# Performance work log

Measured on AMD Instinct MI355X. Metric: run time of the kernel, lower is better.

The kernel has to match this reference:

```python
import jax, jax.numpy as jnp
import numpy as np

B, T, D = 1, 4096, 2048
NUM_HEADS, NUM_KV_HEADS, HEAD_DIM = 16, 8, 128
QUERY_PRE_ATTN_SCALAR = HEAD_DIM ** -0.5
SOFT_CAP = 50.0
WINDOW = 1024
ROPE_BASE = 10000.0
ROPE_SCALE = 1.0
K_MASK = -2.3819763e+38


def apply_rope(x, positions, head_dim, max_wavelength=ROPE_BASE, scale_factor=ROPE_SCALE):
    # x: [B, T, N, H], positions: [B, T]
    fraction = 2.0 * jnp.arange(head_dim // 2, dtype=jnp.float32) / head_dim
    timescale = max_wavelength ** fraction  # [H/2]
    sinusoid = positions[..., None].astype(jnp.float32) / timescale  # [B, T, H/2]
    sinusoid = (sinusoid / scale_factor)[..., None, :]  # [B, T, 1, H/2]
    sin, cos = jnp.sin(sinusoid), jnp.cos(sinusoid)
    first, second = jnp.split(x, 2, axis=-1)
    out = jnp.concatenate([first * cos - second * sin,
                           second * cos + first * sin], axis=-1)
    return out.astype(x.dtype)


def setup_inputs() -> dict:
    key = jax.random.key(0)
    ks = jax.random.split(key, 4)
    x = jax.random.normal(ks[0], (B, T, D), dtype=jnp.float32)
    segment_pos = jnp.broadcast_to(jnp.arange(T, dtype=jnp.int32), (B, T))
    # causal mask [B, T, S]
    attn_mask = jnp.broadcast_to(
        jnp.tril(jnp.ones((T, T), dtype=jnp.bool_)), (B, T, T))
    q_w = jax.random.normal(ks[1], (NUM_HEADS, D, HEAD_DIM), dtype=jnp.float32) * 0.02
    kv_w = jax.random.normal(ks[2], (2, NUM_KV_HEADS, D, HEAD_DIM), dtype=jnp.float32) * 0.02
    o_w = jax.random.normal(ks[3], (NUM_HEADS, HEAD_DIM, D), dtype=jnp.float32) * 0.02
    return {"x": x, "segment_pos": segment_pos, "attn_mask": attn_mask,
            "q_w": q_w, "kv_w": kv_w, "o_w": o_w}


def reference(x, segment_pos, attn_mask, q_w, kv_w, o_w):
    # Projections (GQA: separate q and kv einsums)
    q = jnp.einsum('BTD,NDH->BTNH', x, q_w)          # [B,T,N,H]
    k = jnp.einsum('BSD,KDH->BSKH', x, kv_w[0])      # [B,S,K,H]
    v = jnp.einsum('BSD,KDH->BSKH', x, kv_w[1])      # [B,S,K,H]

    q = apply_rope(q, segment_pos, HEAD_DIM)
    q = q * QUERY_PRE_ATTN_SCALAR
    k = apply_rope(k, segment_pos, HEAD_DIM)

    num_groups = NUM_HEADS // NUM_KV_HEADS
    qg = q.reshape(B, T, NUM_KV_HEADS, num_groups, HEAD_DIM)
    logits = jnp.einsum('BTKGH,BSKH->BTKGS', qg, k)
    logits = logits.reshape(B, T, NUM_HEADS, -1)     # [B,T,N,S]

    # soft cap
    logits = jnp.tanh(logits / SOFT_CAP) * SOFT_CAP

    # sliding-window mask combined with causal mask
    all_ones = jnp.ones_like(attn_mask)
    sliding = jnp.triu(all_ones, -WINDOW + 1) * jnp.tril(all_ones, WINDOW - 1)
    mask = sliding * attn_mask                       # [B,T,S] bool

    padded = jnp.where(mask[:, :, None, :], logits, K_MASK)
    probs = jax.nn.softmax(padded, axis=-1).astype(k.dtype)

    probs_g = probs.reshape(B, T, NUM_KV_HEADS, num_groups, -1)
    encoded = jnp.einsum('BTKGS,BSKH->BTKGH', probs_g, v)
    encoded = encoded.reshape(B, T, NUM_HEADS, HEAD_DIM)

    attn_output = jnp.einsum('BTNH,NHD->BTD', encoded, o_w)
    return attn_output
```

## Files before the change

kernel.cpp:

```cpp
#include <hip/hip_runtime.h>
#include <hip/hip_bf16.h>
#include <math.h>

typedef __attribute__((ext_vector_type(8))) short short8;
typedef __attribute__((ext_vector_type(8))) unsigned short ushort8;
typedef __attribute__((ext_vector_type(4))) float f32x4;

#define T_SEQ 4096
#define D_MODEL 2048
#define N_HEADS 16
#define N_KV 8
#define HEAD_DIM 128
#define QSCALE 0.08838834764831845f

__device__ __forceinline__ float bf2f(unsigned short u) {
  union { unsigned int i; float f; } x; x.i = ((unsigned int)u) << 16; return x.f;
}
__device__ __forceinline__ unsigned short f2bf(float f) {
  union { float f; unsigned int i; } x; x.f = f;
  unsigned int i = x.i;
  unsigned int r = i + 0x7fffu + ((i >> 16) & 1u);
  return (unsigned short)(r >> 16);
}

__global__ __launch_bounds__(256) void cvt_x_kernel(const float* __restrict__ x,
                                                    unsigned short* __restrict__ xb) {
  int idx = blockIdx.x * 256 + threadIdx.x;
  const float4* p = reinterpret_cast<const float4*>(x) + (size_t)idx * 2;
  float4 a = p[0], b = p[1];
  ushort8 o;
  o[0] = f2bf(a.x); o[1] = f2bf(a.y); o[2] = f2bf(a.z); o[3] = f2bf(a.w);
  o[4] = f2bf(b.x); o[5] = f2bf(b.y); o[6] = f2bf(b.z); o[7] = f2bf(b.w);
  reinterpret_cast<ushort8*>(xb)[idx] = o;
}

__global__ __launch_bounds__(256) void rope_table_kernel(const int* __restrict__ segpos,
                                                         float2* __restrict__ tab) {
  int idx = blockIdx.x * 256 + threadIdx.x;
  int t = idx >> 6, i = idx & 63;
  float pos = (float)segpos[t];
  float ts = powf(10000.f, (float)(2 * i) / 128.f);
  float ang = pos / ts;
  tab[idx] = make_float2(sinf(ang), cosf(ang));
}

__global__ __launch_bounds__(256) void transpose_f32_bf16_kernel(const float* __restrict__ src,
                                                                 unsigned short* __restrict__ dst,
                                                                 int sstride, int dstride,
                                                                 long sBatch, long dBatch) {
  __shared__ float tile[32][33];
  long b = blockIdx.z;
  src += b * sBatch; dst += b * dBatch;
  int c0 = blockIdx.x * 32, r0 = blockIdx.y * 32;
  int tx = threadIdx.x & 31, ty = threadIdx.x >> 5;
#pragma unroll
  for (int i = 0; i < 4; ++i)
    tile[ty + i * 8][tx] = src[(size_t)(r0 + ty + i * 8) * sstride + c0 + tx];
  __syncthreads();
#pragma unroll
  for (int i = 0; i < 4; ++i)
    dst[(size_t)(c0 + ty + i * 8) * dstride + r0 + tx] = f2bf(tile[tx][ty + i * 8]);
}

__global__ __launch_bounds__(256) void transpose_bf16_kernel(const unsigned short* __restrict__ src,
                                                             unsigned short* __restrict__ dst,
                                                             int sstride, int dstride,
                                                             long sBatch, long dBatch) {
  __shared__ unsigned short tile[32][33];
  long b = blockIdx.z;
  src += b * sBatch; dst += b * dBatch;
  int c0 = blockIdx.x * 32, r0 = blockIdx.y * 32;
  int tx = threadIdx.x & 31, ty = threadIdx.x >> 5;
#pragma unroll
  for (int i = 0; i < 4; ++i)
    tile[ty + i * 8][tx] = src[(size_t)(r0 + ty + i * 8) * sstride + c0 + tx];
  __syncthreads();
#pragma unroll
  for (int i = 0; i < 4; ++i)
    dst[(size_t)(c0 + ty + i * 8) * dstride + r0 + tx] = tile[tx][ty + i * 8];
}

#define G2L(gp, lp)                                                           \
  __builtin_amdgcn_global_load_lds(                                           \
      (const __attribute__((address_space(1))) void*)(gp),                    \
      (__attribute__((address_space(3))) void*)(lp), 16, 0, 0)

template <int OUT_BF16>
__global__ __launch_bounds__(256) void gemm_bt_kernel(const unsigned short* __restrict__ A,
                                                      const unsigned short* __restrict__ Bt,
                                                      void* __restrict__ Cout,
                                                      int M, int N, int K) {
  __shared__ unsigned short As[2][128 * 64];
  __shared__ unsigned short Bs[2][128 * 64];
  const int tid = threadIdx.x;
  const int lane = tid & 63;
  const int wave = tid >> 6;
  const int lr = lane & 15, lg = lane >> 4;
  const long brow = (long)blockIdx.y * 128, bcol = (long)blockIdx.x * 128;
  const int wr = (wave >> 1) * 64, wc = (wave & 1) * 64;
  f32x4 acc[4][4] = {};

  const int er = tid >> 3;
  const int ecs = ((tid & 7) * 8) ^ ((er & 7) << 3);
  const unsigned short* gA = A + (size_t)(brow + er) * K + ecs;
  const unsigned short* gB = Bt + (size_t)(bcol + er) * K + ecs;
  const int ldst = wave * 512;

#define STAGE(buf, k0)                                                        \
  {                                                                           \
    _Pragma("unroll")                                                         \
    for (int i = 0; i < 4; ++i) {                                             \
      G2L(gA + (size_t)i * 32 * K + (k0), &As[buf][i * 2048 + ldst]);         \
      G2L(gB + (size_t)i * 32 * K + (k0), &Bs[buf][i * 2048 + ldst]);         \
    }                                                                         \
  }

  const int nk = K >> 6;
  STAGE(0, 0);
  asm volatile("s_waitcnt vmcnt(0)" ::: "memory");
  __syncthreads();
  int cur = 0;
  const int swr = (lr & 7) << 3;
  for (int t = 0; t < nk; ++t) {
    if (t + 1 < nk) STAGE(cur ^ 1, (t + 1) << 6);
#pragma unroll
    for (int kk = 0; kk < 64; kk += 32) {
      short8 af[4], bfr[4];
#pragma unroll
      for (int m = 0; m < 4; ++m)
        af[m] = *(const short8*)&As[cur][(wr + m * 16 + lr) * 64 + ((kk + lg * 8) ^ swr)];
#pragma unroll
      for (int n = 0; n < 4; ++n)
        bfr[n] = *(const short8*)&Bs[cur][(wc + n * 16 + lr) * 64 + ((kk + lg * 8) ^ swr)];
#pragma unroll
      for (int m = 0; m < 4; ++m)
#pragma unroll
        for (int n = 0; n < 4; ++n)
          acc[m][n] = __builtin_amdgcn_mfma_f32_16x16x32_bf16(af[m], bfr[n], acc[m][n], 0, 0, 0);
    }
    asm volatile("s_waitcnt vmcnt(0)" ::: "memory");
    __syncthreads();
    cur ^= 1;
  }
#undef STAGE

#pragma unroll
  for (int m = 0; m < 4; ++m) {
#pragma unroll
    for (int i = 0; i < 4; ++i) {
      long row = brow + wr + m * 16 + lg * 4 + i;
#pragma unroll
      for (int n = 0; n < 4; ++n) {
        long col = bcol + wc + n * 16 + lr;
        if (OUT_BF16)
          ((unsigned short*)Cout)[row * N + col] = f2bf(acc[m][n][i]);
        else
          ((float*)Cout)[row * N + col] = acc[m][n][i];
      }
    }
  }
}

__global__ __launch_bounds__(256) void rope_apply_kernel(const unsigned short* __restrict__ raw,
                                                         const float2* __restrict__ tab,
                                                         unsigned short* __restrict__ Qb,
                                                         unsigned short* __restrict__ Kb) {
  int gid = blockIdx.x * 256 + threadIdx.x;
  int j = gid & 7;
  int rem = gid >> 3;
  int hs = rem % 24;
  int t = rem / 24;
  int i0 = j * 8;
  float sv[8], cv[8];
  const float2* tp = tab + t * 64 + i0;
#pragma unroll
  for (int q = 0; q < 8; ++q) { float2 sc2 = tp[q]; sv[q] = sc2.x; cv[q] = sc2.y; }
  if (hs < 16) {
    const unsigned short* p = raw + (size_t)t * 4096 + hs * 128 + i0;
    ushort8 a = *(const ushort8*)p;
    ushort8 b = *(const ushort8*)(p + 64);
    ushort8 o1, o2;
#pragma unroll
    for (int q = 0; q < 8; ++q) {
      float fa = bf2f(a[q]), fb = bf2f(b[q]);
      o1[q] = f2bf((fa * cv[q] - fb * sv[q]) * QSCALE);
      o2[q] = f2bf((fb * cv[q] + fa * sv[q]) * QSCALE);
    }
    unsigned short* qp = Qb + ((size_t)hs * T_SEQ + t) * 128 + i0;
    *(ushort8*)qp = o1;
    *(ushort8*)(qp + 64) = o2;
  } else {
    int kn = hs - 16;
    const unsigned short* p = raw + (size_t)t * 4096 + 2048 + kn * 128 + i0;
    ushort8 a = *(const ushort8*)p;
    ushort8 b = *(const ushort8*)(p + 64);
    ushort8 o1, o2;
#pragma unroll
    for (int q = 0; q < 8; ++q) {
      float fa = bf2f(a[q]), fb = bf2f(b[q]);
      o1[q] = f2bf(fa * cv[q] - fb * sv[q]);
      o2[q] = f2bf(fb * cv[q] + fa * sv[q]);
    }
    unsigned short* kp = Kb + ((size_t)kn * T_SEQ + t) * 128 + i0;
    *(ushort8*)kp = o1;
    *(ushort8*)(kp + 64) = o2;
  }
}

__global__ __launch_bounds__(512) void attn_kernel(const unsigned short* __restrict__ Qb,
                                                   const unsigned short* __restrict__ Kb,
                                                   const unsigned short* __restrict__ Vt,
                                                   unsigned short* __restrict__ enc) {
  __shared__ unsigned short Ks[64][128];
  __shared__ unsigned short Vs[128][64];
  __shared__ unsigned short Ps[8][16][66];
  int lin = blockIdx.y * 32 + blockIdx.x;
  lin = (lin & 7) * 64 + (lin >> 3);
  const int h = lin >> 5;
  const int qb0 = (lin & 31) * 128;
  const int kvh = h >> 1;
  const int tid = threadIdx.x, lane = tid & 63, wave = tid >> 6;
  const int qw = qb0 + wave * 16;
  const int lr = lane & 15, lg = lane >> 4;
  const int sw = (lr & 7) << 3;

  short8 aq[4];
  {
    const unsigned short* qp = Qb + ((size_t)h * T_SEQ + qw + lr) * 128 + lg * 8;
#pragma unroll
    for (int c = 0; c < 4; ++c) aq[c] = *(const short8*)(qp + c * 32);
  }
  f32x4 acc[8] = {};
  float lsum[4] = {0.f, 0.f, 0.f, 0.f};

  const int s_lo = (qb0 - 1023) > 0 ? (qb0 - 1023) : 0;
  const int kb_lo = s_lo >> 6, kb_hi = (qb0 + 127) >> 6;

  const int rK = tid >> 4;
  const int cpK = (tid & 15) * 8;
  const int colK = cpK ^ ((rK & 7) << 3);
  const int rV = tid >> 3;
  const int cpV = (tid & 7) * 8;
  const int colV = cpV ^ ((rV & 7) << 3);
  const unsigned short* kgb = Kb + ((size_t)kvh * T_SEQ + rK) * 128 + colK;
  const unsigned short* vgb = Vt + ((size_t)kvh * 128 + rV) * T_SEQ + colV;

  ushort8 kr0, kr1, vr0, vr1;
  {
    const int s0g = kb_lo * 64;
    kr0 = *(const ushort8*)(kgb + (size_t)s0g * 128);
    kr1 = *(const ushort8*)(kgb + (size_t)(s0g + 32) * 128);
    vr0 = *(const ushort8*)(vgb + s0g);
    vr1 = *(const ushort8*)(vgb + (size_t)64 * T_SEQ + s0g);
  }

  for (int kb = kb_lo; kb <= kb_hi; ++kb) {
    const int s0g = kb * 64;
    __syncthreads();
    *(ushort8*)&Ks[rK][cpK] = kr0;
    *(ushort8*)&Ks[rK + 32][cpK] = kr1;
    *(ushort8*)&Vs[rV][cpV] = vr0;
    *(ushort8*)&Vs[rV + 64][cpV] = vr1;
    __syncthreads();
    if (kb < kb_hi) {
      const int sn = s0g + 64;
      kr0 = *(const ushort8*)(kgb + (size_t)sn * 128);
      kr1 = *(const ushort8*)(kgb + (size_t)(sn + 32) * 128);
      vr0 = *(const ushort8*)(vgb + sn);
      vr1 = *(const ushort8*)(vgb + (size_t)64 * T_SEQ + sn);
    }
    if (s0g > qw + 15 || s0g + 63 < qw - 1023) continue;

    f32x4 sv[4] = {};
#pragma unroll
    for (int st = 0; st < 4; ++st) {
      const int krow = st * 16 + lr;
#pragma unroll
      for (int c = 0; c < 4; ++c) {
        short8 b = *(const short8*)&Ks[krow][(c * 32 + lg * 8) ^ sw];
        sv[st] = __builtin_amdgcn_mfma_f32_16x16x32_bf16(aq[c], b, sv[st], 0, 0, 0);
      }
    }
#pragma unroll
    for (int st = 0; st < 4; ++st) {
#pragma unroll
      for (int r = 0; r < 4; ++r) {
        float s = sv[st][r];
        float z2 = s * s * 4.0e-4f;
        float capped = s * (15.f + z2) * __builtin_amdgcn_rcpf(fmaf(z2, 6.f, 15.f));
        float p = __expf(capped);
        int qg = qw + lg * 4 + r;
        int sg = s0g + st * 16 + lr;
        p = ((unsigned)(qg - sg) <= 1023u) ? p : 0.f;
        lsum[r] += p;
        Ps[wave][lg * 4 + r][st * 16 + lr] = f2bf(p);
      }
    }
    short8 pa0 = *(const short8*)&Ps[wave][lr][lg * 8];
    short8 pa1 = *(const short8*)&Ps[wave][lr][32 + lg * 8];
#pragma unroll
    for (int d0 = 0; d0 < 8; ++d0) {
      const int vrow = d0 * 16 + lr;
      short8 bv0 = *(const short8*)&Vs[vrow][(lg * 8) ^ sw];
      short8 bv1 = *(const short8*)&Vs[vrow][(32 + lg * 8) ^ sw];
      acc[d0] = __builtin_amdgcn_mfma_f32_16x16x32_bf16(pa0, bv0, acc[d0], 0, 0, 0);
      acc[d0] = __builtin_amdgcn_mfma_f32_16x16x32_bf16(pa1, bv1, acc[d0], 0, 0, 0);
    }
  }

#pragma unroll
  for (int r = 0; r < 4; ++r) {
    float l = lsum[r];
    l += __shfl_xor(l, 1);
    l += __shfl_xor(l, 2);
    l += __shfl_xor(l, 4);
    l += __shfl_xor(l, 8);
    float inv = __builtin_amdgcn_rcpf(l);
    int row = qw + lg * 4 + r;
    unsigned short* op = enc + (size_t)row * D_MODEL + h * 128 + lr;
#pragma unroll
    for (int d0 = 0; d0 < 8; ++d0) op[d0 * 16] = f2bf(acc[d0][r] * inv);
  }
}

extern "C" void kernel_launch(void* const* d_in, const int* in_sizes, int n_in,
                              void* d_out, int out_size, void* d_ws, size_t ws_size,
                              hipStream_t stream) {
  const float* x = (const float*)d_in[0];
  const int* segpos = (const int*)d_in[1];
  const float* q_w = (const float*)d_in[3];
  const float* kv_w = (const float*)d_in[4];
  const float* o_w = (const float*)d_in[5];
  float* out = (float*)d_out;
  char* ws = (char*)d_ws;

  const size_t OFF_XB = 0;
  const size_t OFF_WT = OFF_XB + 16777216;
  const size_t OFF_RAW = OFF_WT + 16777216;
  const size_t OFF_KB = OFF_RAW + 33554432;
  const size_t OFF_VT = OFF_KB + 8388608;
  const size_t OFF_TAB = OFF_VT + 8388608;
  unsigned short* xb = (unsigned short*)(ws + OFF_XB);
  unsigned short* Wt = (unsigned short*)(ws + OFF_WT);
  unsigned short* raw = (unsigned short*)(ws + OFF_RAW);
  unsigned short* Kb = (unsigned short*)(ws + OFF_KB);
  unsigned short* Vt = (unsigned short*)(ws + OFF_VT);
  float2* tab = (float2*)(ws + OFF_TAB);
  unsigned short* o_wt = xb;
  unsigned short* Qb = Wt;
  unsigned short* enc = raw;

  cvt_x_kernel<<<dim3(4096), dim3(256), 0, stream>>>(x, xb);
  rope_table_kernel<<<dim3(1024), dim3(256), 0, stream>>>(segpos, tab);
  transpose_f32_bf16_kernel<<<dim3(4, 64, 16), dim3(256), 0, stream>>>(
      q_w, Wt, 128, 2048, (long)2048 * 128, (long)128 * 2048);
  transpose_f32_bf16_kernel<<<dim3(4, 64, 16), dim3(256), 0, stream>>>(
      kv_w, Wt + (size_t)2048 * 2048, 128, 2048, (long)2048 * 128, (long)128 * 2048);
  gemm_bt_kernel<1><<<dim3(32, 32), dim3(256), 0, stream>>>(xb, Wt, (void*)raw, 4096, 4096, 2048);
  transpose_f32_bf16_kernel<<<dim3(64, 64, 1), dim3(256), 0, stream>>>(
      o_w, o_wt, 2048, 2048, 0L, 0L);
  rope_apply_kernel<<<dim3(3072), dim3(256), 0, stream>>>(raw, tab, Qb, Kb);
  transpose_bf16_kernel<<<dim3(4, 128, 8), dim3(256), 0, stream>>>(
      raw + 3072, Vt, 4096, 4096, 128L, (long)128 * 4096);
  attn_kernel<<<dim3(32, 16), dim3(512), 0, stream>>>(Qb, Kb, Vt, enc);
  gemm_bt_kernel<0><<<dim3(16, 32), dim3(256), 0, stream>>>(enc, o_wt, (void*)out, 4096, 2048, 2048);
}
```

Measured before the change: 224.5 us.

## Replace 128x128 GEMM with 256x256 tile, 8-wave pipelined GEMM and block swizzle

Replaces the two projection GEMMs with a 256x256-tile kernel of 512 threads, using 128KB dynamic LDS with double buffering. Loads are interleaved with MFMA phases using explicit barriers, vmcnt waits and setprio. Block IDs are swizzled for L2 locality. The goal is higher arithmetic intensity and better latency hiding, at the cost of fewer blocks: 256 and 128 workgroups on 256 CUs, which risks underfilling the GPU for the output projection.

After: 226.9 us. No clear change (+1.0%).

```diff
diff --git a/kernel.cpp b/kernel.cpp
--- a/kernel.cpp
+++ b/kernel.cpp
@@ -84,74 +84,126 @@
   __builtin_amdgcn_global_load_lds(                                           \
       (const __attribute__((address_space(1))) void*)(gp),                    \
       (__attribute__((address_space(3))) void*)(lp), 16, 0, 0)
+#define GBAR() asm volatile("s_barrier" ::: "memory")
+#define VMW(n) asm volatile("s_waitcnt vmcnt(" #n ")" ::: "memory")
 
 template <int OUT_BF16>
-__global__ __launch_bounds__(256) void gemm_bt_kernel(const unsigned short* __restrict__ A,
-                                                      const unsigned short* __restrict__ Bt,
-                                                      void* __restrict__ Cout,
-                                                      int M, int N, int K) {
-  __shared__ unsigned short As[2][128 * 64];
-  __shared__ unsigned short Bs[2][128 * 64];
+__global__ __launch_bounds__(512, 2) void gemm256_kernel(const unsigned short* __restrict__ A,
+                                                         const unsigned short* __restrict__ Bt,
+                                                         void* __restrict__ Cout,
+                                                         int M, int N, int K) {
+  extern __shared__ unsigned short smem[];
+  unsigned short* ldsA = smem;
+  unsigned short* ldsB = smem + 32768;
   const int tid = threadIdx.x;
-  const int lane = tid & 63;
-  const int wave = tid >> 6;
+  const int lane = tid & 63, wave = tid >> 6;
+  const int wm = wave >> 2, wn = wave & 3;
   const int lr = lane & 15, lg = lane >> 4;
-  const long brow = (long)blockIdx.y * 128, bcol = (long)blockIdx.x * 128;
-  const int wr = (wave >> 1) * 64, wc = (wave & 1) * 64;
-  f32x4 acc[4][4] = {};
-
-  const int er = tid >> 3;
-  const int ecs = ((tid & 7) * 8) ^ ((er & 7) << 3);
-  const unsigned short* gA = A + (size_t)(brow + er) * K + ecs;
-  const unsigned short* gB = Bt + (size_t)(bcol + er) * K + ecs;
-  const int ldst = wave * 512;
-
-#define STAGE(buf, k0)                                                        \
-  {                                                                           \
+  const int swz = (lr & 7) << 3;
+  const int c0s = (lg * 8) ^ swz;
+  const int c1s = (32 + lg * 8) ^ swz;
+
+  int id = blockIdx.y * gridDim.x + blockIdx.x;
+  int nb = gridDim.x * gridDim.y;
+  int sw = (id & 7) * (nb >> 3) + (id >> 3);
+  const long brow = (long)(sw / gridDim.x) * 256;
+  const long bcol = (long)(sw % gridDim.x) * 256;
+
+  const unsigned short* Ag = A + brow * K;
+  const unsigned short* Bg = Bt + bcol * K;
+
+  const int r0 = tid >> 3;
+  const int cs = ((tid & 7) * 8) ^ ((r0 & 7) << 3);
+
+#define ST_A(tt, b, a)                                                        \
+  { G2L(Ag + (size_t)((a) * 128 + r0) * K + (size_t)(tt) * 64 + cs,           \
+        ldsA + (b) * 16384 + (a) * 8192 + tid * 8);                           \
+    G2L(Ag + (size_t)((a) * 128 + r0 + 64) * K + (size_t)(tt) * 64 + cs,      \
+        ldsA + (b) * 16384 + (a) * 8192 + 4096 + tid * 8); }
+#define ST_B(tt, b, h)                                                        \
+  { G2L(Bg + (size_t)((h) * 128 + r0) * K + (size_t)(tt) * 64 + cs,           \
+        ldsB + (b) * 16384 + (h) * 8192 + tid * 8);                           \
+    G2L(Bg + (size_t)((h) * 128 + r0 + 64) * K + (size_t)(tt) * 64 + cs,      \
+        ldsB + (b) * 16384 + (h) * 8192 + 4096 + tid * 8); }
+
+  f32x4 acc[8][4] = {};
+  short8 bf[4][2];
+  short8 af[4];
+
+#define RD_B(b)                                                               \
+  { const unsigned short* pb = ldsB + (b) * 16384 + (wn >> 1) * 8192 + (wn & 1) * 4096; \
     _Pragma("unroll")                                                         \
-    for (int i = 0; i < 4; ++i) {                                             \
-      G2L(gA + (size_t)i * 32 * K + (k0), &As[buf][i * 2048 + ldst]);         \
-      G2L(gB + (size_t)i * 32 * K + (k0), &Bs[buf][i * 2048 + ldst]);         \
+    for (int n = 0; n < 4; ++n) {                                             \
+      bf[n][0] = *(const short8*)(pb + (n * 16 + lr) * 64 + c0s);             \
+      bf[n][1] = *(const short8*)(pb + (n * 16 + lr) * 64 + c1s);             \
+    } }
+#define RD_A(b, mb)                                                           \
+  { const unsigned short* pa = ldsA + (b) * 16384 + wm * 8192;                \
+    af[0] = *(const short8*)(pa + ((mb) * 16 + lr) * 64 + c0s);               \
+    af[1] = *(const short8*)(pa + ((mb) * 16 + lr) * 64 + c1s);               \
+    af[2] = *(const short8*)(pa + ((mb) * 16 + 16 + lr) * 64 + c0s);          \
+    af[3] = *(const short8*)(pa + ((mb) * 16 + 16 + lr) * 64 + c1s); }
+#define MFMA2(mb)                                                             \
+  { __builtin_amdgcn_s_setprio(1);                                            \
+    _Pragma("unroll")                                                         \
+    for (int n = 0; n < 4; ++n) {                                             \
+      acc[mb][n]     = __builtin_amdgcn_mfma_f32_16x16x32_bf16(af[0], bf[n][0], acc[mb][n], 0, 0, 0);     \
+      acc[mb][n]     = __builtin_amdgcn_mfma_f32_16x16x32_bf16(af[1], bf[n][1], acc[mb][n], 0, 0, 0);     \
+      acc[mb + 1][n] = __builtin_amdgcn_mfma_f32_16x16x32_bf16(af[2], bf[n][0], acc[mb + 1][n], 0, 0, 0); \
+      acc[mb + 1][n] = __builtin_amdgcn_mfma_f32_16x16x32_bf16(af[3], bf[n][1], acc[mb + 1][n], 0, 0, 0); \
     }                                                                         \
-  }
-
-  const int nk = K >> 6;
-  STAGE(0, 0);
-  asm volatile("s_waitcnt vmcnt(0)" ::: "memory");
-  __syncthreads();
-  int cur = 0;
-  const int swr = (lr & 7) << 3;
-  for (int t = 0; t < nk; ++t) {
-    if (t + 1 < nk) STAGE(cur ^ 1, (t + 1) << 6);
-#pragma unroll
-    for (int kk = 0; kk < 64; kk += 32) {
-      short8 af[4], bfr[4];
-#pragma unroll
-      for (int m = 0; m < 4; ++m)
-        af[m] = *(const short8*)&As[cur][(wr + m * 16 + lr) * 64 + ((kk + lg * 8) ^ swr)];
-#pragma unroll
-      for (int n = 0; n < 4; ++n)
-        bfr[n] = *(const short8*)&Bs[cur][(wc + n * 16 + lr) * 64 + ((kk + lg * 8) ^ swr)];
-#pragma unroll
-      for (int m = 0; m < 4; ++m)
-#pragma unroll
-        for (int n = 0; n < 4; ++n)
-          acc[m][n] = __builtin_amdgcn_mfma_f32_16x16x32_bf16(af[m], bfr[n], acc[m][n], 0, 0, 0);
-    }
-    asm volatile("s_waitcnt vmcnt(0)" ::: "memory");
-    __syncthreads();
-    cur ^= 1;
-  }
-#undef STAGE
-
-#pragma unroll
-  for (int m = 0; m < 4; ++m) {
+    __builtin_amdgcn_s_setprio(0); }
+
+  ST_B(0, 0, 0); ST_B(0, 0, 1); ST_A(0, 0, 0); ST_A(0, 0, 1);
+  ST_B(1, 1, 0); ST_B(1, 1, 1);
+  VMW(4);
+  ST_A(1, 1, 0); ST_A(1, 1, 1);
+  GBAR();
+
+  const int NT = K >> 6;
+  for (int j = 0; j < (NT >> 1); ++j) {
+    const int t2 = 2 * j + 2, t3 = 2 * j + 3;
+    const bool s2 = t2 < NT, s3 = t3 < NT;
+    RD_B(0); RD_A(0, 0);
+    if (s2) ST_B(t2, 0, 0);
+    GBAR(); MFMA2(0); GBAR();
+    RD_A(0, 2);
+    if (s2) ST_B(t2, 0, 1);
+    GBAR(); MFMA2(2); GBAR();
+    RD_A(0, 4);
+    GBAR(); MFMA2(4); GBAR();
+    RD_A(0, 6);
+    if (s2) { VMW(4); ST_A(t2, 0, 0); ST_A(t2, 0, 1); }
+    else    { VMW(0); }
+    GBAR(); MFMA2(6); GBAR();
+    RD_B(1); RD_A(1, 0);
+    if (s3) ST_B(t3, 1, 0);
+    GBAR(); MFMA2(0); GBAR();
+    RD_A(1, 2);
+    if (s3) ST_B(t3, 1, 1);
+    GBAR(); MFMA2(2); GBAR();
+    RD_A(1, 4);
+    GBAR(); MFMA2(4); GBAR();
+    RD_A(1, 6);
+    if (s3) { VMW(4); ST_A(t3, 1, 0); ST_A(t3, 1, 1); }
+    else    { VMW(0); }
+    GBAR(); MFMA2(6); GBAR();
+  }
+
+#undef ST_A
+#undef ST_B
+#undef RD_A
+#undef RD_B
+#undef MFMA2
+
+#pragma unroll
+  for (int m = 0; m < 8; ++m) {
 #pragma unroll
     for (int i = 0; i < 4; ++i) {
-      long row = brow + wr + m * 16 + lg * 4 + i;
+      long row = brow + wm * 128 + m * 16 + lg * 4 + i;
 #pragma unroll
       for (int n = 0; n < 4; ++n) {
-        long col = bcol + wc + n * 16 + lr;
+        long col = bcol + wn * 64 + n * 16 + lr;
         if (OUT_BF16)
           ((unsigned short*)Cout)[row * N + col] = f2bf(acc[m][n][i]);
         else
@@ -350,18 +402,23 @@
   unsigned short* Qb = Wt;
   unsigned short* enc = raw;
 
+  hipFuncSetAttribute((const void*)(gemm256_kernel<1>),
+                      hipFuncAttributeMaxDynamicSharedMemorySize, 131072);
+  hipFuncSetAttribute((const void*)(gemm256_kernel<0>),
+                      hipFuncAttributeMaxDynamicSharedMemorySize, 131072);
+
   cvt_x_kernel<<<dim3(4096), dim3(256), 0, stream>>>(x, xb);
   rope_table_kernel<<<dim3(1024), dim3(256), 0, stream>>>(segpos, tab);
   transpose_f32_bf16_kernel<<<dim3(4, 64, 16), dim3(256), 0, stream>>>(
       q_w, Wt, 128, 2048, (long)2048 * 128, (long)128 * 2048);
   transpose_f32_bf16_kernel<<<dim3(4, 64, 16), dim3(256), 0, stream>>>(
       kv_w, Wt + (size_t)2048 * 2048, 128, 2048, (long)2048 * 128, (long)128 * 2048);
-  gemm_bt_kernel<1><<<dim3(32, 32), dim3(256), 0, stream>>>(xb, Wt, (void*)raw, 4096, 4096, 2048);
+  gemm256_kernel<1><<<dim3(16, 16), dim3(512), 131072, stream>>>(xb, Wt, (void*)raw, 4096, 4096, 2048);
   transpose_f32_bf16_kernel<<<dim3(64, 64, 1), dim3(256), 0, stream>>>(
       o_w, o_wt, 2048, 2048, 0L, 0L);
   rope_apply_kernel<<<dim3(3072), dim3(256), 0, stream>>>(raw, tab, Qb, Kb);
   transpose_bf16_kernel<<<dim3(4, 128, 8), dim3(256), 0, stream>>>(
       raw + 3072, Vt, 4096, 4096, 128L, (long)128 * 4096);
   attn_kernel<<<dim3(32, 16), dim3(512), 0, stream>>>(Qb, Kb, Vt, enc);
-  gemm_bt_kernel<0><<<dim3(16, 32), dim3(256), 0, stream>>>(enc, o_wt, (void*)out, 4096, 2048, 2048);
-}
+  gemm256_kernel<0><<<dim3(8, 16), dim3(512), 131072, stream>>>(enc, o_wt, (void*)out, 4096, 2048, 2048);
+}
```
